# Kernel optimization log

Hardware: AMD Instinct MI355X
Metric: run time of the kernel (lower is better)

## Reference

```python
import jax, jax.numpy as jnp
import numpy as np

DIM = 512
HEADS = 8
DIM_HEAD = 64
BLOCKS = 6
EXCHANGES = 3
EPS = 1.1920929e-07  # torch.finfo(float32).eps used by RMSNorm(eps=None)


def _rmsnorm(x, w):
    return x * jax.lax.rsqrt(jnp.mean(x * x, axis=-1, keepdims=True) + EPS) * w


def _attention(x, ctx, nw, wq, wkv, wo):
    # x: [B, i, d] queries; ctx: [B, j, d] context (NOT normalized, as in original)
    B = x.shape[0]
    xn = _rmsnorm(x, nw)
    q = jnp.einsum('bid,ed->bie', xn, wq)
    kv = jnp.einsum('bjd,ed->bje', ctx, wkv)
    k, v = jnp.split(kv, 2, axis=-1)
    heads = lambda t: t.reshape(B, t.shape[1], HEADS, DIM_HEAD).transpose(0, 2, 1, 3)
    q, k, v = heads(q), heads(k), heads(v)
    sim = jnp.einsum('bhid,bhjd->bhij', q, k)  # NOTE: original never applies self.scale
    attn = jax.nn.softmax(sim, axis=-1)
    out = jnp.einsum('bhij,bhjd->bhid', attn, v)
    out = out.transpose(0, 2, 1, 3).reshape(B, -1, HEADS * DIM_HEAD)
    return jnp.einsum('bie,de->bid', out, wo)


def _feedforward(x, nw, kw, kb, vw, vb):
    q = _rmsnorm(x, nw)
    h = jnp.einsum('...d,ed->...e', q, kw) + kb
    sim, gates = jnp.split(h, 2, axis=-1)
    h = sim * jax.nn.gelu(gates, approximate=False)  # F.gelu default = exact erf
    return jnp.einsum('...e,de->...d', h, vw) + vb


def _forward(tokens, attn_norm_w, attn_wq, attn_wkv, attn_wo,
             ff_norm_w, ff_keys_w, ff_keys_b, ff_values_w, ff_values_b,
             res_norm_w, res_wq, res_wkv, res_wo):
    b, n, d = tokens.shape
    tokens = jnp.broadcast_to(tokens[None], (BLOCKS, b, n, d))
    messages = [tokens]
    for _ in range(EXCHANGES):
        flat = tokens.reshape(BLOCKS * b, n, d)
        attended = _attention(flat, flat, attn_norm_w, attn_wq, attn_wkv, attn_wo)
        attended = attended.reshape(BLOCKS, b, n, d)
        retrieved = _feedforward(tokens, ff_norm_w, ff_keys_w, ff_keys_b, ff_values_w, ff_values_b)
        messages += [attended, retrieved]
        packed = jnp.concatenate(messages, axis=0)           # [M, b, n, d]
        M = packed.shape[0]
        # einops: repeat 'm b n d -> (b blocks) n m d'
        ctx = jnp.broadcast_to(packed.transpose(1, 2, 0, 3)[:, None], (b, BLOCKS, n, M, d))
        ctx = ctx.reshape(b * BLOCKS * n, M, d)
        # queries packed '(blocks b) n d' then '* n d' -> [blocks*b*n, 1, d]
        q = tokens.reshape(BLOCKS * b * n, 1, d)
        pooled = _attention(q, ctx, res_norm_w, res_wq, res_wkv, res_wo)
        tokens = pooled.reshape(BLOCKS, b, n, d)
    return tokens


def setup_inputs() -> dict:
    key = jax.random.key(0)
    ks = jax.random.split(key, 12)
    b, n, d = 2, 256, DIM
    di = HEADS * DIM_HEAD
    dff = int(d * 4.0 * 2 / 3)
    s = lambda k, shp, fan: (jax.random.normal(k, shp, jnp.float32) / np.sqrt(fan)).astype(jnp.float32)
    return {
        'tokens': jax.random.normal(ks[0], (b, n, d), jnp.float32),
        'attn_norm_w': 1.0 + 0.05 * jax.random.normal(ks[1], (d,), jnp.float32),
        'attn_wq': s(ks[2], (di, d), d),
        'attn_wkv': s(ks[3], (2 * di, d), d),
        'attn_wo': s(ks[4], (d, di), di),
        'ff_norm_w': 1.0 + 0.05 * jax.random.normal(ks[5], (d,), jnp.float32),
        'ff_keys_w': s(ks[6], (2 * dff, d), d),
        'ff_keys_b': 0.01 * jax.random.normal(ks[7], (2 * dff,), jnp.float32),
        'ff_values_w': s(ks[8], (d, dff), dff),
        'ff_values_b': 0.01 * jax.random.normal(ks[9], (d,), jnp.float32),
        'res_norm_w': 1.0 + 0.05 * jax.random.normal(ks[10], (d,), jnp.float32),
        'res_wq': s(ks[11], (di, d), d),
        'res_wkv': s(jax.random.fold_in(key, 100), (2 * di, d), d),
        'res_wo': s(jax.random.fold_in(key, 101), (d, di), di),
    }


def reference(tokens, attn_norm_w, attn_wq, attn_wkv, attn_wo,
              ff_norm_w, ff_keys_w, ff_keys_b, ff_values_w, ff_values_b,
              res_norm_w, res_wq, res_wkv, res_wo):
    return _forward(tokens, attn_norm_w, attn_wq, attn_wkv, attn_wo,
                    ff_norm_w, ff_keys_w, ff_keys_b, ff_values_w, ff_values_b,
                    res_norm_w, res_wq, res_wkv, res_wo)
```

## Files before the change

kernel.cpp:

```cpp
#include <hip/hip_runtime.h>
#include <math.h>

#define Dm   512
#define Nn_  256
#define Bv   2
#define NTD  1024
#define NH   8
#define DH   64
#define DFF  1365
#define DFF2 2730
#define KFF  1408
#define NFF  2816
#define NMD  14
#define EPSR 1.1920929e-07f

typedef _Float16 h16;
typedef h16  v8h  __attribute__((ext_vector_type(8)));
typedef float v4f __attribute__((ext_vector_type(4)));

__device__ inline h16 f2h(float v) { return (h16)v; }

__device__ inline void glds16(const void* g, void* l) {
    __builtin_amdgcn_global_load_lds((const __attribute__((address_space(1))) void*)g,
                                     (__attribute__((address_space(3))) void*)l, 16, 0, 0);
}

struct GDesc {
    const h16* A;
    const h16* W;
    const float* bias;
    float* C;
    h16* Cbf;
    long Apl, Wpl, bfpl;
    int lda, ldw, ldc, Nd, mbase, K, mode, nbx;
};

template <int BM>
__global__ __launch_bounds__(256) void mega_gemm(GDesc d0, GDesc d1, GDesc d2, GDesc d3,
                                                 int n0, int n01, int n012)
{
    constexpr int MI = BM / 32;
    constexpr int ASEG = BM / 16;
    constexpr int NSEG = 2 * ASEG + 16;
    constexpr int BUF = 2 * BM * 32 + 2 * 4096;
    constexpr int AH = 0, AL = BM * 32, WH = 2 * BM * 32, WL = 2 * BM * 32 + 4096;
    __shared__ h16 lds[2 * BUF];

    GDesc d; int lb = blockIdx.x;
    if (lb < n0) d = d0;
    else if (lb < n01) { d = d1; lb -= n0; }
    else if (lb < n012) { d = d2; lb -= n01; }
    else { d = d3; lb -= n012; }
    const int bx = lb % d.nbx;
    const int by = lb / d.nbx;

    const int tid = threadIdx.x;
    const int wid = tid >> 6;
    const int lane = tid & 63;
    const int wm = wid >> 1, wn = wid & 1;
    const int row16 = lane & 15, quad = lane >> 4;
    const long i0 = (long)bx * BM;
    const long j0 = (long)by * 128;
    const int l4 = lane >> 2;
    const int l2s = ((lane & 3) ^ (l4 & 3)) * 8;
    const int ksw = (quad ^ (row16 & 3)) * 8;

    auto stage = [&](int k0, h16* buf) {
        #pragma unroll
        for (int s = 0; s < NSEG / 4; ++s) {
            const int sg = wid * (NSEG / 4) + s;
            const h16* src;
            int dst;
            if (sg < ASEG) {
                src = d.A + (i0 + sg * 16 + l4) * (long)d.lda + k0 + l2s;
                dst = AH + sg * 512;
            } else if (sg < 2 * ASEG) {
                const int r = sg - ASEG;
                src = d.A + d.Apl + (i0 + r * 16 + l4) * (long)d.lda + k0 + l2s;
                dst = AL + r * 512;
            } else if (sg < 2 * ASEG + 8) {
                const int r = sg - 2 * ASEG;
                src = d.W + (j0 + r * 16 + l4) * (long)d.ldw + k0 + l2s;
                dst = WH + r * 512;
            } else {
                const int r = sg - 2 * ASEG - 8;
                src = d.W + d.Wpl + (j0 + r * 16 + l4) * (long)d.ldw + k0 + l2s;
                dst = WL + r * 512;
            }
            glds16(src, &buf[dst]);
        }
    };

    v4f acc[MI][4];
    #pragma unroll
    for (int a = 0; a < MI; ++a)
        #pragma unroll
        for (int b = 0; b < 4; ++b) acc[a][b] = (v4f){0.f, 0.f, 0.f, 0.f};

    stage(0, lds);
    int cur = 0;
    for (int k0 = 0; k0 < d.K; k0 += 32) {
        __syncthreads();
        h16* cbuf = &lds[cur * BUF];
        if (k0 + 32 < d.K) stage(k0 + 32, &lds[(cur ^ 1) * BUF]);

        v8h af[MI], al[MI];
        #pragma unroll
        for (int mi = 0; mi < MI; ++mi) {
            const int aoff = (wm * (BM / 2) + mi * 16 + row16) * 32 + ksw;
            af[mi] = *(const v8h*)&cbuf[AH + aoff];
            al[mi] = *(const v8h*)&cbuf[AL + aoff];
        }
        #pragma unroll
        for (int nj = 0; nj < 4; ++nj) {
            const int boff = (wn * 64 + nj * 16 + row16) * 32 + ksw;
            v8h bh = *(const v8h*)&cbuf[WH + boff];
            v8h bl = *(const v8h*)&cbuf[WL + boff];
            #pragma unroll
            for (int mi = 0; mi < MI; ++mi) {
                acc[mi][nj] = __builtin_amdgcn_mfma_f32_16x16x32_f16(af[mi], bh, acc[mi][nj], 0, 0, 0);
                acc[mi][nj] = __builtin_amdgcn_mfma_f32_16x16x32_f16(af[mi], bl, acc[mi][nj], 0, 0, 0);
                acc[mi][nj] = __builtin_amdgcn_mfma_f32_16x16x32_f16(al[mi], bh, acc[mi][nj], 0, 0, 0);
            }
        }
        cur ^= 1;
    }

    #pragma unroll
    for (int nj = 0; nj < 4; ++nj) {
        const int col = (int)j0 + wn * 64 + nj * 16 + row16;
        if (col < d.Nd) {
            const float bv = d.bias ? d.bias[col] : 0.f;
            #pragma unroll
            for (int mi = 0; mi < MI; ++mi) {
                #pragma unroll
                for (int r = 0; r < 4; ++r) {
                    const long row = i0 + wm * (BM / 2) + mi * 16 + quad * 4 + r;
                    const float v = acc[mi][nj][r] + bv;
                    if (d.mode == 0) {
                        d.C[row * (long)d.ldc + col] = v;
                    } else if (d.mode == 1) {
                        const long idx = row * (long)d.ldc + col;
                        const h16 hi = f2h(v);
                        d.Cbf[idx] = hi; d.Cbf[idx + d.bfpl] = f2h(v - (float)hi);
                    } else if (d.mode == 2) {
                        const long idx = row * (long)d.ldc + col;
                        d.C[idx] = v;
                        const h16 hi = f2h(v);
                        d.Cbf[idx] = hi; d.Cbf[idx + d.bfpl] = f2h(v - (float)hi);
                    } else if (d.mode == 3) {
                        const int rr = (int)row & 1023;
                        const int md = d.mbase * 2 + (rr >> 9);
                        const long orow = (long)(((rr >> 8) & 1) * 256 + (rr & 255)) * NMD + md;
                        d.C[orow * 1024 + col] = v;
                    } else if (d.mode == 4) {
                        const h16 hi = f2h(v);
                        const h16 lo = f2h(v - (float)hi);
                        if (col < 512) {
                            const long idx = row * 512 + col;
                            d.Cbf[idx] = hi; d.Cbf[idx + d.bfpl] = lo;
                        } else {
                            const int c = col - 512;
                            const int bh_ = ((int)(row >> 8)) * 8 + (c >> 6);
                            const long idx = (((long)bh_ * 64 + (c & 63)) << 8) + (row & 255);
                            h16* vtp = (h16*)d.C;
                            vtp[idx] = hi; vtp[idx + d.bfpl] = lo;
                        }
                    } else {
                        const int g = (int)(row >> 9), bb = ((int)row >> 8) & 1, nn = (int)row & 255;
                        #pragma unroll
                        for (int rep = 0; rep < 3; ++rep) {
                            const long orow = (long)(((g * 3 + rep) * 2 + bb) * 256 + nn);
                            d.C[orow * (long)d.ldc + col] = v;
                        }
                    }
                }
            }
        }
    }
}

__global__ void cvt_hilo(const float* __restrict__ x, int Ms, int Ks, int Kp,
                         h16* __restrict__ y, long plane, int total)
{
    const int idx = blockIdx.x * 256 + threadIdx.x;
    if (idx >= total) return;
    const int row = idx / Kp;
    const int col = idx - row * Kp;
    const float v = (row < Ms && col < Ks) ? x[(long)row * Ks + col] : 0.f;
    const h16 hi = f2h(v);
    y[idx] = hi;
    y[idx + plane] = f2h(v - (float)hi);
}

__global__ void cvt_hilo_T(const float* __restrict__ x, int R, int C,
                           h16* __restrict__ y, long plane, int total)
{
    const int idx = blockIdx.x * 256 + threadIdx.x;
    if (idx >= total) return;
    const int row = idx / R;
    const int col = idx - row * R;
    const float v = (row < C) ? x[(long)col * C + row] : 0.f;
    const h16 hi = f2h(v);
    y[idx] = hi;
    y[idx + plane] = f2h(v - (float)hi);
}

__global__ void fold_bias(const float* __restrict__ wkv, const float* __restrict__ b,
                          float* __restrict__ out)
{
    const int n = blockIdx.x * 256 + threadIdx.x;
    if (n >= 1024) return;
    float s = 0.f;
    const float* row = wkv + (long)n * 512;
    for (int d2 = 0; d2 < 512; ++d2) s = fmaf(row[d2], b[d2], s);
    out[n] = s;
}

__global__ __launch_bounds__(256) void rmsnorm3_bf(
    const float* __restrict__ x,
    const float* __restrict__ w0, const float* __restrict__ w1,
    const float* __restrict__ w2,
    h16* __restrict__ y0, h16* __restrict__ y1,
    h16* __restrict__ y2, long plane)
{
    const int r = blockIdx.x;
    const float* xr = x + (long)r * Dm;
    const int t = threadIdx.x;
    const float a = xr[t];
    const float b = xr[t + 256];
    float ss = a * a + b * b;
    #pragma unroll
    for (int off = 32; off > 0; off >>= 1) ss += __shfl_xor(ss, off, 64);
    __shared__ float w4[4];
    if ((t & 63) == 0) w4[t >> 6] = ss;
    __syncthreads();
    const float rs = rsqrtf((w4[0] + w4[1] + w4[2] + w4[3]) * (1.f / 512.f) + EPSR);
    const float na = a * rs, nb = b * rs;
    const long ia = (long)r * Dm + t, ib = ia + 256;
    h16 h;
    float v;
    v = na * w0[t];       h = f2h(v); y0[ia] = h; y0[ia + plane] = f2h(v - (float)h);
    v = nb * w0[t + 256]; h = f2h(v); y0[ib] = h; y0[ib + plane] = f2h(v - (float)h);
    v = na * w1[t];       h = f2h(v); y1[ia] = h; y1[ia + plane] = f2h(v - (float)h);
    v = nb * w1[t + 256]; h = f2h(v); y1[ib] = h; y1[ib + plane] = f2h(v - (float)h);
    v = na * w2[t];       h = f2h(v); y2[ia] = h; y2[ia + plane] = f2h(v - (float)h);
    v = nb * w2[t + 256]; h = f2h(v); y2[ib] = h; y2[ib + plane] = f2h(v - (float)h);
}

__global__ __launch_bounds__(256) void attn_glu(
    const h16* __restrict__ qhl, const h16* __restrict__ khl,
    const h16* __restrict__ vtb, long pl, h16* __restrict__ outbf,
    const float* __restrict__ hbuf, h16* __restrict__ hbf, long hpl)
{
    if (blockIdx.x >= 128) {
        const int r = blockIdx.x - 128;
        const float* row = hbuf + (long)r * NFF;
        for (int c = threadIdx.x; c < KFF; c += 256) {
            float v = 0.f;
            if (c < DFF) {
                const float sim = row[c];
                const float g = row[c + DFF];
                v = sim * (0.5f * g * (1.f + erff(g * 0.70710678118654752440f)));
            }
            const long idx = (long)r * KFF + c;
            const h16 hi = f2h(v);
            hbf[idx] = hi;
            hbf[idx + hpl] = f2h(v - (float)hi);
        }
        return;
    }

    __shared__ h16 kh[4096], kl[4096], vh[4096], vl[4096];
    __shared__ h16 pH[4 * 1024], pL[4 * 1024];

    const int bat = blockIdx.x >> 5;
    const int head = (blockIdx.x >> 2) & 7;
    const int qc = blockIdx.x & 3;
    const int t = threadIdx.x;
    const int w = t >> 6, lane = t & 63;
    const int row16 = lane & 15, quad = lane >> 4;

    v8h qh[2], ql[2];
    {
        const long qrow = (long)bat * 256 + qc * 64 + w * 16 + row16;
        const h16* qp = qhl + qrow * 512 + head * 64 + quad * 8;
        qh[0] = *(const v8h*)qp;        qh[1] = *(const v8h*)(qp + 32);
        ql[0] = *(const v8h*)(qp + pl); ql[1] = *(const v8h*)(qp + pl + 32);
    }

    v4f O[4];
    #pragma unroll
    for (int i = 0; i < 4; ++i) O[i] = (v4f){0.f, 0.f, 0.f, 0.f};
    float m[4] = {-1e30f, -1e30f, -1e30f, -1e30f};
    float l[4] = {0.f, 0.f, 0.f, 0.f};

    const int sj = t >> 3;
    const int sc = t & 7;
    const long kbase = ((long)bat * 256) * 512 + head * 64;
    const long vbase = ((long)(bat * 8 + head) * 64) << 8;

    for (int jc = 0; jc < 256; jc += 64) {
        __syncthreads();
        #pragma unroll
        for (int rep = 0; rep < 2; ++rep) {
            const int row = sj + rep * 32;
            const int dsw = row * 64 + ((sc ^ (row & 7)) * 8);
            const h16* ks = khl + kbase + (long)(jc + row) * 512 + sc * 8;
            const h16* vs = vtb + vbase + ((long)row << 8) + jc + sc * 8;
            *(v8h*)&kh[dsw] = *(const v8h*)ks;
            *(v8h*)&kl[dsw] = *(const v8h*)(ks + pl);
            *(v8h*)&vh[dsw] = *(const v8h*)vs;
            *(v8h*)&vl[dsw] = *(const v8h*)(vs + pl);
        }
        __syncthreads();

        v4f S[4];
        #pragma unroll
        for (int i = 0; i < 4; ++i) S[i] = (v4f){0.f, 0.f, 0.f, 0.f};
        #pragma unroll
        for (int kk = 0; kk < 2; ++kk) {
            #pragma unroll
            for (int tile = 0; tile < 4; ++tile) {
                const int off = (tile * 16 + row16) * 64 + (((kk * 4 + quad) ^ (row16 & 7)) * 8);
                v8h bh = *(const v8h*)&kh[off];
                v8h bl = *(const v8h*)&kl[off];
                S[tile] = __builtin_amdgcn_mfma_f32_16x16x32_f16(qh[kk], bh, S[tile], 0, 0, 0);
                S[tile] = __builtin_amdgcn_mfma_f32_16x16x32_f16(qh[kk], bl, S[tile], 0, 0, 0);
                S[tile] = __builtin_amdgcn_mfma_f32_16x16x32_f16(ql[kk], bh, S[tile], 0, 0, 0);
            }
        }

        float mc[4], sums[4], alpha[4];
        #pragma unroll
        for (int r = 0; r < 4; ++r) {
            float v = fmaxf(fmaxf(S[0][r], S[1][r]), fmaxf(S[2][r], S[3][r]));
            v = fmaxf(v, __shfl_xor(v, 1, 64));
            v = fmaxf(v, __shfl_xor(v, 2, 64));
            v = fmaxf(v, __shfl_xor(v, 4, 64));
            v = fmaxf(v, __shfl_xor(v, 8, 64));
            mc[r] = v;
        }
        #pragma unroll
        for (int r = 0; r < 4; ++r) {
            const float mn = fmaxf(m[r], mc[r]);
            alpha[r] = __expf(m[r] - mn);
            m[r] = mn;
            sums[r] = 0.f;
        }
        #pragma unroll
        for (int tile = 0; tile < 4; ++tile) {
            #pragma unroll
            for (int r = 0; r < 4; ++r) {
                const float p = __expf(S[tile][r] - m[r]);
                S[tile][r] = p;
                sums[r] += p;
            }
        }
        #pragma unroll
        for (int r = 0; r < 4; ++r) {
            float v = sums[r];
            v += __shfl_xor(v, 1, 64);
            v += __shfl_xor(v, 2, 64);
            v += __shfl_xor(v, 4, 64);
            v += __shfl_xor(v, 8, 64);
            l[r] = l[r] * alpha[r] + v;
        }
        #pragma unroll
        for (int tile = 0; tile < 4; ++tile)
            #pragma unroll
            for (int r = 0; r < 4; ++r) O[tile][r] *= alpha[r];

        #pragma unroll
        for (int tile = 0; tile < 4; ++tile) {
            const int chunkcol = tile * 2 + (row16 >> 3);
            #pragma unroll
            for (int r = 0; r < 4; ++r) {
                const int prow = quad * 4 + r;
                const int addr = w * 1024 + prow * 64 +
                                 ((chunkcol ^ (prow & 7)) * 8) + (row16 & 7);
                const float p = S[tile][r];
                const h16 hi = f2h(p);
                pH[addr] = hi;
                pL[addr] = f2h(p - (float)hi);
            }
        }

        #pragma unroll
        for (int kk = 0; kk < 2; ++kk) {
            const int poff = w * 1024 + row16 * 64 + (((kk * 4 + quad) ^ (row16 & 7)) * 8);
            v8h pa = *(const v8h*)&pH[poff];
            v8h pb = *(const v8h*)&pL[poff];
            #pragma unroll
            for (int tile = 0; tile < 4; ++tile) {
                const int off = (tile * 16 + row16) * 64 + (((kk * 4 + quad) ^ (row16 & 7)) * 8);
                v8h vbh = *(const v8h*)&vh[off];
                v8h vbl = *(const v8h*)&vl[off];
                O[tile] = __builtin_amdgcn_mfma_f32_16x16x32_f16(pa, vbh, O[tile], 0, 0, 0);
                O[tile] = __builtin_amdgcn_mfma_f32_16x16x32_f16(pa, vbl, O[tile], 0, 0, 0);
                O[tile] = __builtin_amdgcn_mfma_f32_16x16x32_f16(pb, vbh, O[tile], 0, 0, 0);
            }
        }
    }

    #pragma unroll
    for (int tile = 0; tile < 4; ++tile) {
        const int dim = tile * 16 + row16;
        #pragma unroll
        for (int r = 0; r < 4; ++r) {
            const long grow = (long)bat * 256 + qc * 64 + w * 16 + quad * 4 + r;
            const float v = O[tile][r] / l[r];
            const long idx = grow * 512 + head * 64 + dim;
            const h16 hi = f2h(v);
            outbf[idx] = hi;
            outbf[idx + pl] = f2h(v - (float)hi);
        }
    }
}

template <int M>
__global__ __launch_bounds__(128) void attn_pool_kernel(
    const float* __restrict__ qb, const float* __restrict__ kvc3,
    h16* __restrict__ outbf, long plane)
{
    const int rb = blockIdx.x >> 3;
    const int h = blockIdx.x & 7;
    __shared__ float k_lds[M * 66];
    __shared__ float v_lds[M * 66];
    __shared__ float q_lds[2 * 64];
    __shared__ float p_lds[2 * 64];
    const int t = threadIdx.x;
    const int g = rb >> 8, nn = rb & 255;

    for (int idx = t; idx < M * 64; idx += 128) {
        const int m = idx >> 6, d = idx & 63;
        const long base = ((long)rb * NMD + m) * 1024 + h * DH + d;
        k_lds[m * 66 + d] = kvc3[base];
        v_lds[m * 66 + d] = kvc3[base + 512];
    }
    {
        const int w = t >> 6, dd = t & 63;
        const long iq = (long)(g * 2 + w) * 256 + nn;
        q_lds[t] = qb[iq * Dm + h * DH + dd];
    }
    __syncthreads();

    const int w = t >> 6;
    const int lane = t & 63;
    float s = -1e30f;
    if (lane < M) {
        s = 0.f;
        const float* kr = &k_lds[lane * 66];
        const float* qr = &q_lds[w * 64];
        #pragma unroll
        for (int dd = 0; dd < 64; dd += 2) {
            s = fmaf(qr[dd], kr[dd], s);
            s = fmaf(qr[dd + 1], kr[dd + 1], s);
        }
    }
    float mx = s;
    #pragma unroll
    for (int off = 32; off > 0; off >>= 1) mx = fmaxf(mx, __shfl_xor(mx, off, 64));
    const float p = __expf(s - mx);
    float l = p;
    #pragma unroll
    for (int off = 32; off > 0; off >>= 1) l += __shfl_xor(l, off, 64);
    p_lds[w * 64 + lane] = p / l;

    float o = 0.f;
    const float* pr = &p_lds[w * 64];
    #pragma unroll
    for (int m = 0; m < M; ++m)
        o = fmaf(pr[m], v_lds[m * 66 + lane], o);

    const long iq = (long)(g * 2 + w) * 256 + nn;
    const long oidx = iq * Dm + h * DH + lane;
    const h16 hi = f2h(o);
    outbf[oidx] = hi;
    outbf[oidx + plane] = f2h(o - (float)hi);
}

__global__ void replicate_kernel(const float* __restrict__ src,
                                 float* __restrict__ tokens,
                                 h16* __restrict__ tokbf, long tpl)
{
    const int idx = blockIdx.x * blockDim.x + threadIdx.x;
    if (idx >= NTD * Dm) return;
    const float v = src[idx & (Bv * Nn_ * Dm - 1)];
    tokens[idx] = v;
    const h16 hi = f2h(v);
    tokbf[idx] = hi;
    tokbf[idx + tpl] = f2h(v - (float)hi);
}

extern "C" void kernel_launch(void* const* d_in, const int* in_sizes, int n_in,
                              void* d_out, int out_size, void* d_ws, size_t ws_size,
                              hipStream_t stream)
{
    const float* tok_in       = (const float*)d_in[0];
    const float* attn_norm_w  = (const float*)d_in[1];
    const float* attn_wq      = (const float*)d_in[2];
    const float* attn_wkv     = (const float*)d_in[3];
    const float* attn_wo      = (const float*)d_in[4];
    const float* ff_norm_w    = (const float*)d_in[5];
    const float* ff_keys_w    = (const float*)d_in[6];
    const float* ff_keys_b    = (const float*)d_in[7];
    const float* ff_values_w  = (const float*)d_in[8];
    const float* ff_values_b  = (const float*)d_in[9];
    const float* res_norm_w   = (const float*)d_in[10];
    const float* res_wq       = (const float*)d_in[11];
    const float* res_wkv      = (const float*)d_in[12];
    const float* res_wo       = (const float*)d_in[13];

    float* ws = (float*)d_ws;
    float* kvc3   = ws;
    float* tokens = kvc3 + 512L * NMD * 1024;
    float* qbuf   = tokens + (long)NTD * Dm;
    float* hbuf   = qbuf + (long)NTD * Dm;
    float* biasWf = hbuf + (long)NTD * NFF;

    h16* us = (h16*)(biasWf + 1024);
    const long apl = (long)NTD * Dm;
    const long hpl = (long)NTD * KFF;
    const long vtpl = (long)NTD * Dm;
    const long w1 = 512L * 512, w2 = 1024L * 512, w3 = (long)NFF * 512;
    const long w5 = (long)KFF * 512;
    const long wa_pl = 1024L * 512;
    const long wf_pl = 1024L * KFF;
    h16* tokbf = us; us += 2 * apl;
    h16* xa    = us; us += 2 * apl;
    h16* xf    = us; us += 2 * apl;
    h16* xr    = us; us += 2 * apl;
    h16* abf   = us; us += 2 * apl;
    h16* hbf   = us; us += 2 * hpl;
    h16* qhl   = us; us += 2 * apl;
    h16* khl   = us; us += 2 * apl;
    h16* vtb   = us; us += 2 * vtpl;
    h16* wqb   = us; us += 2 * w1;
    h16* wkvb  = us; us += 2 * w2;
    h16* fkb   = us; us += 2 * w3;
    h16* rqb   = us; us += 2 * w1;
    h16* rkvb  = us; us += 2 * w2;
    h16* rob   = us; us += 2 * w1;
    h16* woTb  = us; us += 2 * w1;
    h16* fvwTb = us; us += 2 * w5;
    h16* Wab   = us; us += 2 * wa_pl;
    h16* Wfb   = us; us += 2 * wf_pl;

    auto cvtw = [&](const float* src, int Ms, int Ks, int Kp, int Mpad,
                    h16* dst, long pl) {
        const int tot = Mpad * Kp;
        cvt_hilo<<<(tot + 255) / 256, 256, 0, stream>>>(src, Ms, Ks, Kp, dst, pl, tot);
    };
    cvtw(attn_wq,   512,  512, 512, 512,  wqb,  w1);
    cvtw(attn_wkv,  1024, 512, 512, 1024, wkvb, w2);
    cvtw(ff_keys_w, DFF2, 512, 512, NFF,  fkb,  w3);
    cvtw(res_wq,    512,  512, 512, 512,  rqb,  w1);
    cvtw(res_wkv,   1024, 512, 512, 1024, rkvb, w2);
    cvtw(res_wo,    512,  512, 512, 512,  rob,  w1);
    cvt_hilo_T<<<(512 * 512 + 255) / 256, 256, 0, stream>>>(attn_wo, 512, 512, woTb, w1, 512 * 512);
    cvt_hilo_T<<<((int)w5 + 255) / 256, 256, 0, stream>>>(ff_values_w, 512, DFF, fvwTb, w5, (int)w5);
    fold_bias<<<4, 256, 0, stream>>>(res_wkv, ff_values_b, biasWf);

    auto mk = [](const h16* A, long Apl, int lda,
                 const h16* W, long Wpl, int ldw,
                 const float* bias, float* C, int ldc, int Nd,
                 h16* Cbf, long bfpl, int mbase, int K,
                 int mode, int nbx) -> GDesc {
        GDesc d;
        d.A = A; d.Apl = Apl; d.lda = lda;
        d.W = W; d.Wpl = Wpl; d.ldw = ldw;
        d.bias = bias; d.C = C; d.ldc = ldc; d.Nd = Nd;
        d.Cbf = Cbf; d.bfpl = bfpl; d.mbase = mbase; d.K = K;
        d.mode = mode; d.nbx = nbx;
        return d;
    };

    {
        GDesc dWf = mk(rkvb, w2, 512, fvwTb, w5, 512, nullptr, nullptr, KFF, KFF,
                       Wfb, wf_pl, 0, 512, 1, 16);
        GDesc dWa = mk(rkvb, w2, 512, woTb, w1, 512, nullptr, nullptr, 512, 512,
                       Wab, wa_pl, 0, 512, 1, 16);
        mega_gemm<64><<<240, 256, 0, stream>>>(dWf, dWa, dWa, dWa, 176, 240, 240);
    }

    replicate_kernel<<<(NTD * Dm + 255) / 256, 256, 0, stream>>>(tok_in, tokens, tokbf, apl);

    for (int e = 0; e < 3; ++e) {
        rmsnorm3_bf<<<NTD, 256, 0, stream>>>(tokens, attn_norm_w, ff_norm_w, res_norm_w,
                                             xa, xf, xr, apl);
        {
            GDesc dffk = mk(xf,    apl, 512, fkb,  w3, 512, ff_keys_b, hbuf, NFF, DFF2,
                            nullptr, 0, 0, 512, 0, 16);
            GDesc dwkv = mk(tokbf, apl, 512, wkvb, w2, 512, nullptr, (float*)vtb, 1024, 1024,
                            khl, apl, 0, 512, 4, 16);
            GDesc dwq  = mk(xa,    apl, 512, wqb,  w1, 512, nullptr, nullptr, 512, 512,
                            qhl, apl, 0, 512, 1, 16);
            mega_gemm<64><<<544, 256, 0, stream>>>(dffk, dwkv, dwq, dwq, 352, 480, 544);
        }
        attn_glu<<<1152, 256, 0, stream>>>(qhl, khl, vtb, apl, abf, hbuf, hbf, hpl);
        {
            GDesc dffvKV = mk(hbf, hpl, KFF, Wfb, wf_pl, KFF, biasWf, kvc3, 1024, 1024,
                              nullptr, 0, 2 + 2 * e, KFF, 3, 16);
            GDesc dwoKV  = mk(abf, apl, 512, Wab, wa_pl, 512, nullptr, kvc3, 1024, 1024,
                              nullptr, 0, 1 + 2 * e, 512, 3, 16);
            GDesc drq    = mk(xr, apl, 512, rqb, w1, 512, nullptr, qbuf, 512, 512,
                              nullptr, 0, 0, 512, 0, 16);
            if (e == 0) {
                GDesc dtokKV = mk(tokbf, apl, 512, rkvb, w2, 512, nullptr, kvc3, 1024, 1024,
                                  nullptr, 0, 0, 512, 3, 16);
                mega_gemm<64><<<448, 256, 0, stream>>>(dffvKV, dwoKV, drq, dtokKV, 128, 256, 320);
            } else {
                mega_gemm<64><<<320, 256, 0, stream>>>(dffvKV, dwoKV, drq, drq, 128, 256, 320);
            }
        }
        if (e == 0)      attn_pool_kernel<6><<<512 * NH, 128, 0, stream>>>(qbuf, kvc3, abf, apl);
        else if (e == 1) attn_pool_kernel<10><<<512 * NH, 128, 0, stream>>>(qbuf, kvc3, abf, apl);
        else             attn_pool_kernel<14><<<512 * NH, 128, 0, stream>>>(qbuf, kvc3, abf, apl);
        {
            if (e < 2) {
                GDesc dro = mk(abf, apl, 512, rob, w1, 512, nullptr, tokens, 512, 512,
                               tokbf, apl, 0, 512, 2, 32);
                mega_gemm<32><<<128, 256, 0, stream>>>(dro, dro, dro, dro, 128, 128, 128);
            } else {
                GDesc dro = mk(abf, apl, 512, rob, w1, 512, nullptr, (float*)d_out, 512, 512,
                               nullptr, 0, 0, 512, 5, 32);
                mega_gemm<32><<<128, 256, 0, stream>>>(dro, dro, dro, dro, 128, 128, 128);
            }
        }
    }
}
```

Baseline: 490.4 us.

## Fold RMSNorm weights into weights, fuse setup kernels, add BN=64 GEMM tiles

The RMSNorm gain vectors are folded into the converted query and FF-key weights. The per-row rsqrt scale is now applied in the GEMM epilogue from a small rs_kernel output, so the three normalized hi/lo activation buffers no longer need to be written and read each exchange. All weight conversion, bias folding and token replication kernels are merged into one setup launch. The GEMM gains a BN template parameter, and most launches use 64x64 tiles with twice as many blocks, which raises parallelism at the cost of reloading the A tile more often.

```diff
diff --git a/kernel.cpp b/kernel.cpp
--- a/kernel.cpp
+++ b/kernel.cpp
@@ -29,21 +29,26 @@
     const h16* A;
     const h16* W;
     const float* bias;
+    const float* rss;
     float* C;
     h16* Cbf;
     long Apl, Wpl, bfpl;
     int lda, ldw, ldc, Nd, mbase, K, mode, nbx;
 };
 
-template <int BM>
+template <int BM, int BN>
 __global__ __launch_bounds__(256) void mega_gemm(GDesc d0, GDesc d1, GDesc d2, GDesc d3,
                                                  int n0, int n01, int n012)
 {
-    constexpr int MI = BM / 32;
+    constexpr int NWN = (BN == 128) ? 2 : 1;
+    constexpr int NWM = 4 / NWN;
+    constexpr int MI = BM / (16 * NWM);
+    constexpr int ABUF = BM * 32;
+    constexpr int WBUFh = BN * 32;
+    constexpr int BUF = 2 * ABUF + 2 * WBUFh;
     constexpr int ASEG = BM / 16;
-    constexpr int NSEG = 2 * ASEG + 16;
-    constexpr int BUF = 2 * BM * 32 + 2 * 4096;
-    constexpr int AH = 0, AL = BM * 32, WH = 2 * BM * 32, WL = 2 * BM * 32 + 4096;
+    constexpr int WSEG = BN / 16;
+    constexpr int NSEG = 2 * ASEG + 2 * WSEG;
     __shared__ h16 lds[2 * BUF];
 
     GDesc d; int lb = blockIdx.x;
@@ -57,10 +62,10 @@
     const int tid = threadIdx.x;
     const int wid = tid >> 6;
     const int lane = tid & 63;
-    const int wm = wid >> 1, wn = wid & 1;
+    const int wm = wid / NWN, wn = wid % NWN;
     const int row16 = lane & 15, quad = lane >> 4;
     const long i0 = (long)bx * BM;
-    const long j0 = (long)by * 128;
+    const long j0 = (long)by * BN;
     const int l4 = lane >> 2;
     const int l2s = ((lane & 3) ^ (l4 & 3)) * 8;
     const int ksw = (quad ^ (row16 & 3)) * 8;
@@ -73,19 +78,19 @@
             int dst;
             if (sg < ASEG) {
                 src = d.A + (i0 + sg * 16 + l4) * (long)d.lda + k0 + l2s;
-                dst = AH + sg * 512;
+                dst = sg * 512;
             } else if (sg < 2 * ASEG) {
                 const int r = sg - ASEG;
                 src = d.A + d.Apl + (i0 + r * 16 + l4) * (long)d.lda + k0 + l2s;
-                dst = AL + r * 512;
-            } else if (sg < 2 * ASEG + 8) {
+                dst = ABUF + r * 512;
+            } else if (sg < 2 * ASEG + WSEG) {
                 const int r = sg - 2 * ASEG;
                 src = d.W + (j0 + r * 16 + l4) * (long)d.ldw + k0 + l2s;
-                dst = WH + r * 512;
+                dst = 2 * ABUF + r * 512;
             } else {
-                const int r = sg - 2 * ASEG - 8;
+                const int r = sg - 2 * ASEG - WSEG;
                 src = d.W + d.Wpl + (j0 + r * 16 + l4) * (long)d.ldw + k0 + l2s;
-                dst = WL + r * 512;
+                dst = 2 * ABUF + WBUFh + r * 512;
             }
             glds16(src, &buf[dst]);
         }
@@ -107,15 +112,15 @@
         v8h af[MI], al[MI];
         #pragma unroll
         for (int mi = 0; mi < MI; ++mi) {
-            const int aoff = (wm * (BM / 2) + mi * 16 + row16) * 32 + ksw;
-            af[mi] = *(const v8h*)&cbuf[AH + aoff];
-            al[mi] = *(const v8h*)&cbuf[AL + aoff];
+            const int aoff = (wm * (16 * MI) + mi * 16 + row16) * 32 + ksw;
+            af[mi] = *(const v8h*)&cbuf[aoff];
+            al[mi] = *(const v8h*)&cbuf[ABUF + aoff];
         }
         #pragma unroll
         for (int nj = 0; nj < 4; ++nj) {
             const int boff = (wn * 64 + nj * 16 + row16) * 32 + ksw;
-            v8h bh = *(const v8h*)&cbuf[WH + boff];
-            v8h bl = *(const v8h*)&cbuf[WL + boff];
+            v8h bh = *(const v8h*)&cbuf[2 * ABUF + boff];
+            v8h bl = *(const v8h*)&cbuf[2 * ABUF + WBUFh + boff];
             #pragma unroll
             for (int mi = 0; mi < MI; ++mi) {
                 acc[mi][nj] = __builtin_amdgcn_mfma_f32_16x16x32_f16(af[mi], bh, acc[mi][nj], 0, 0, 0);
@@ -135,8 +140,10 @@
             for (int mi = 0; mi < MI; ++mi) {
                 #pragma unroll
                 for (int r = 0; r < 4; ++r) {
-                    const long row = i0 + wm * (BM / 2) + mi * 16 + quad * 4 + r;
-                    const float v = acc[mi][nj][r] + bv;
+                    const long row = i0 + wm * (16 * MI) + mi * 16 + quad * 4 + r;
+                    float v = acc[mi][nj][r];
+                    if (d.rss) v *= d.rss[(int)row];
+                    v += bv;
                     if (d.mode == 0) {
                         d.C[row * (long)d.ldc + col] = v;
                     } else if (d.mode == 1) {
@@ -180,24 +187,29 @@
     }
 }
 
-__global__ void cvt_hilo(const float* __restrict__ x, int Ms, int Ks, int Kp,
-                         h16* __restrict__ y, long plane, int total)
-{
-    const int idx = blockIdx.x * 256 + threadIdx.x;
-    if (idx >= total) return;
+struct SetupP {
+    const float *attn_wq, *attn_wkv, *ff_keys_w, *res_wq, *res_wkv, *res_wo,
+                *attn_wo, *ff_values_w, *ff_values_b,
+                *attn_norm_w, *ff_norm_w, *res_norm_w, *tok_in;
+    h16 *wqb, *wkvb, *fkb, *rqb, *rkvb, *rob, *woTb, *fvwTb, *tokbf;
+    float *biasWf, *tokens;
+};
+
+__device__ inline void cvt_dev(int idx, const float* x, int Ms, int Ks, int Kp,
+                               h16* y, long plane, const float* cs)
+{
     const int row = idx / Kp;
     const int col = idx - row * Kp;
-    const float v = (row < Ms && col < Ks) ? x[(long)row * Ks + col] : 0.f;
+    float v = (row < Ms && col < Ks) ? x[(long)row * Ks + col] : 0.f;
+    if (cs) v *= cs[col];
     const h16 hi = f2h(v);
     y[idx] = hi;
     y[idx + plane] = f2h(v - (float)hi);
 }
 
-__global__ void cvt_hilo_T(const float* __restrict__ x, int R, int C,
-                           h16* __restrict__ y, long plane, int total)
-{
-    const int idx = blockIdx.x * 256 + threadIdx.x;
-    if (idx >= total) return;
+__device__ inline void cvtT_dev(int idx, const float* x, int R, int C,
+                                h16* y, long plane)
+{
     const int row = idx / R;
     const int col = idx - row * R;
     const float v = (row < C) ? x[(long)col * C + row] : 0.f;
@@ -206,46 +218,63 @@
     y[idx + plane] = f2h(v - (float)hi);
 }
 
-__global__ void fold_bias(const float* __restrict__ wkv, const float* __restrict__ b,
-                          float* __restrict__ out)
-{
-    const int n = blockIdx.x * 256 + threadIdx.x;
-    if (n >= 1024) return;
-    float s = 0.f;
-    const float* row = wkv + (long)n * 512;
-    for (int d2 = 0; d2 < 512; ++d2) s = fmaf(row[d2], b[d2], s);
-    out[n] = s;
-}
-
-__global__ __launch_bounds__(256) void rmsnorm3_bf(
-    const float* __restrict__ x,
-    const float* __restrict__ w0, const float* __restrict__ w1,
-    const float* __restrict__ w2,
-    h16* __restrict__ y0, h16* __restrict__ y1,
-    h16* __restrict__ y2, long plane)
-{
-    const int r = blockIdx.x;
-    const float* xr = x + (long)r * Dm;
+__global__ __launch_bounds__(256) void setup_all(SetupP p)
+{
+    long b = blockIdx.x;
     const int t = threadIdx.x;
-    const float a = xr[t];
-    const float b = xr[t + 256];
-    float ss = a * a + b * b;
+    if (b < 1024) { cvt_dev((int)(b * 256 + t), p.attn_wq, 512, 512, 512, p.wqb, 512L * 512, p.attn_norm_w); return; }
+    b -= 1024;
+    if (b < 2048) { cvt_dev((int)(b * 256 + t), p.attn_wkv, 1024, 512, 512, p.wkvb, 1024L * 512, nullptr); return; }
+    b -= 2048;
+    if (b < 5632) { cvt_dev((int)(b * 256 + t), p.ff_keys_w, DFF2, 512, 512, p.fkb, (long)NFF * 512, p.ff_norm_w); return; }
+    b -= 5632;
+    if (b < 1024) { cvt_dev((int)(b * 256 + t), p.res_wq, 512, 512, 512, p.rqb, 512L * 512, p.res_norm_w); return; }
+    b -= 1024;
+    if (b < 2048) { cvt_dev((int)(b * 256 + t), p.res_wkv, 1024, 512, 512, p.rkvb, 1024L * 512, nullptr); return; }
+    b -= 2048;
+    if (b < 1024) { cvt_dev((int)(b * 256 + t), p.res_wo, 512, 512, 512, p.rob, 512L * 512, nullptr); return; }
+    b -= 1024;
+    if (b < 1024) { cvtT_dev((int)(b * 256 + t), p.attn_wo, 512, 512, p.woTb, 512L * 512); return; }
+    b -= 1024;
+    if (b < 2816) { cvtT_dev((int)(b * 256 + t), p.ff_values_w, 512, DFF, p.fvwTb, (long)KFF * 512); return; }
+    b -= 2816;
+    if (b < 4) {
+        const int n = (int)(b * 256 + t);
+        if (n < 1024) {
+            float s = 0.f;
+            const float* row = p.res_wkv + (long)n * 512;
+            for (int dd = 0; dd < 512; ++dd) s = fmaf(row[dd], p.ff_values_b[dd], s);
+            p.biasWf[n] = s;
+        }
+        return;
+    }
+    b -= 4;
+    {
+        const int idx = (int)(b * 256 + t);
+        const float v = p.tok_in[idx & (Bv * Nn_ * Dm - 1)];
+        p.tokens[idx] = v;
+        const h16 hi = f2h(v);
+        p.tokbf[idx] = hi;
+        p.tokbf[idx + (long)NTD * Dm] = f2h(v - (float)hi);
+    }
+}
+#define SETUP_BLOCKS 18692
+
+__global__ __launch_bounds__(256) void rs_kernel(const float* __restrict__ x,
+                                                 float* __restrict__ rs)
+{
+    const int r = blockIdx.x * 4 + (threadIdx.x >> 6);
+    const int lane = threadIdx.x & 63;
+    const float* row = x + (long)r * Dm + lane * 8;
+    float ss = 0.f;
+    #pragma unroll
+    for (int i = 0; i < 8; i += 4) {
+        const float4 v = *(const float4*)(row + i);
+        ss += v.x * v.x + v.y * v.y + v.z * v.z + v.w * v.w;
+    }
     #pragma unroll
     for (int off = 32; off > 0; off >>= 1) ss += __shfl_xor(ss, off, 64);
-    __shared__ float w4[4];
-    if ((t & 63) == 0) w4[t >> 6] = ss;
-    __syncthreads();
-    const float rs = rsqrtf((w4[0] + w4[1] + w4[2] + w4[3]) * (1.f / 512.f) + EPSR);
-    const float na = a * rs, nb = b * rs;
-    const long ia = (long)r * Dm + t, ib = ia + 256;
-    h16 h;
-    float v;
-    v = na * w0[t];       h = f2h(v); y0[ia] = h; y0[ia + plane] = f2h(v - (float)h);
-    v = nb * w0[t + 256]; h = f2h(v); y0[ib] = h; y0[ib + plane] = f2h(v - (float)h);
-    v = na * w1[t];       h = f2h(v); y1[ia] = h; y1[ia + plane] = f2h(v - (float)h);
-    v = nb * w1[t + 256]; h = f2h(v); y1[ib] = h; y1[ib + plane] = f2h(v - (float)h);
-    v = na * w2[t];       h = f2h(v); y2[ia] = h; y2[ia + plane] = f2h(v - (float)h);
-    v = nb * w2[t + 256]; h = f2h(v); y2[ib] = h; y2[ib + plane] = f2h(v - (float)h);
+    if (lane == 0) rs[r] = rsqrtf(ss * (1.f / 512.f) + EPSR);
 }
 
 __global__ __launch_bounds__(256) void attn_glu(
@@ -478,19 +507,6 @@
     const h16 hi = f2h(o);
     outbf[oidx] = hi;
     outbf[oidx + plane] = f2h(o - (float)hi);
-}
-
-__global__ void replicate_kernel(const float* __restrict__ src,
-                                 float* __restrict__ tokens,
-                                 h16* __restrict__ tokbf, long tpl)
-{
-    const int idx = blockIdx.x * blockDim.x + threadIdx.x;
-    if (idx >= NTD * Dm) return;
-    const float v = src[idx & (Bv * Nn_ * Dm - 1)];
-    tokens[idx] = v;
-    const h16 hi = f2h(v);
-    tokbf[idx] = hi;
-    tokbf[idx + tpl] = f2h(v - (float)hi);
 }
 
 extern "C" void kernel_launch(void* const* d_in, const int* in_sizes, int n_in,
@@ -518,24 +534,21 @@
     float* qbuf   = tokens + (long)NTD * Dm;
     float* hbuf   = qbuf + (long)NTD * Dm;
     float* biasWf = hbuf + (long)NTD * NFF;
-
-    h16* us = (h16*)(biasWf + 1024);
+    float* rsbuf  = biasWf + 1024;
+
+    h16* us = (h16*)(rsbuf + 1024);
     const long apl = (long)NTD * Dm;
     const long hpl = (long)NTD * KFF;
-    const long vtpl = (long)NTD * Dm;
     const long w1 = 512L * 512, w2 = 1024L * 512, w3 = (long)NFF * 512;
     const long w5 = (long)KFF * 512;
     const long wa_pl = 1024L * 512;
     const long wf_pl = 1024L * KFF;
     h16* tokbf = us; us += 2 * apl;
-    h16* xa    = us; us += 2 * apl;
-    h16* xf    = us; us += 2 * apl;
-    h16* xr    = us; us += 2 * apl;
     h16* abf   = us; us += 2 * apl;
     h16* hbf   = us; us += 2 * hpl;
     h16* qhl   = us; us += 2 * apl;
     h16* khl   = us; us += 2 * apl;
-    h16* vtb   = us; us += 2 * vtpl;
+    h16* vtb   = us; us += 2 * apl;
     h16* wqb   = us; us += 2 * w1;
     h16* wkvb  = us; us += 2 * w2;
     h16* fkb   = us; us += 2 * w3;
@@ -547,71 +560,67 @@
     h16* Wab   = us; us += 2 * wa_pl;
     h16* Wfb   = us; us += 2 * wf_pl;
 
-    auto cvtw = [&](const float* src, int Ms, int Ks, int Kp, int Mpad,
-                    h16* dst, long pl) {
-        const int tot = Mpad * Kp;
-        cvt_hilo<<<(tot + 255) / 256, 256, 0, stream>>>(src, Ms, Ks, Kp, dst, pl, tot);
-    };
-    cvtw(attn_wq,   512,  512, 512, 512,  wqb,  w1);
-    cvtw(attn_wkv,  1024, 512, 512, 1024, wkvb, w2);
-    cvtw(ff_keys_w, DFF2, 512, 512, NFF,  fkb,  w3);
-    cvtw(res_wq,    512,  512, 512, 512,  rqb,  w1);
-    cvtw(res_wkv,   1024, 512, 512, 1024, rkvb, w2);
-    cvtw(res_wo,    512,  512, 512, 512,  rob,  w1);
-    cvt_hilo_T<<<(512 * 512 + 255) / 256, 256, 0, stream>>>(attn_wo, 512, 512, woTb, w1, 512 * 512);
-    cvt_hilo_T<<<((int)w5 + 255) / 256, 256, 0, stream>>>(ff_values_w, 512, DFF, fvwTb, w5, (int)w5);
-    fold_bias<<<4, 256, 0, stream>>>(res_wkv, ff_values_b, biasWf);
+    {
+        SetupP p;
+        p.attn_wq = attn_wq; p.attn_wkv = attn_wkv; p.ff_keys_w = ff_keys_w;
+        p.res_wq = res_wq; p.res_wkv = res_wkv; p.res_wo = res_wo;
+        p.attn_wo = attn_wo; p.ff_values_w = ff_values_w; p.ff_values_b = ff_values_b;
+        p.attn_norm_w = attn_norm_w; p.ff_norm_w = ff_norm_w; p.res_norm_w = res_norm_w;
+        p.tok_in = tok_in;
+        p.wqb = wqb; p.wkvb = wkvb; p.fkb = fkb; p.rqb = rqb; p.rkvb = rkvb;
+        p.rob = rob; p.woTb = woTb; p.fvwTb = fvwTb; p.tokbf = tokbf;
+        p.biasWf = biasWf; p.tokens = tokens;
+        setup_all<<<SETUP_BLOCKS, 256, 0, stream>>>(p);
+    }
 
     auto mk = [](const h16* A, long Apl, int lda,
                  const h16* W, long Wpl, int ldw,
-                 const float* bias, float* C, int ldc, int Nd,
+                 const float* bias, const float* rss,
+                 float* C, int ldc, int Nd,
                  h16* Cbf, long bfpl, int mbase, int K,
                  int mode, int nbx) -> GDesc {
         GDesc d;
         d.A = A; d.Apl = Apl; d.lda = lda;
         d.W = W; d.Wpl = Wpl; d.ldw = ldw;
-        d.bias = bias; d.C = C; d.ldc = ldc; d.Nd = Nd;
+        d.bias = bias; d.rss = rss; d.C = C; d.ldc = ldc; d.Nd = Nd;
         d.Cbf = Cbf; d.bfpl = bfpl; d.mbase = mbase; d.K = K;
         d.mode = mode; d.nbx = nbx;
         return d;
     };
 
     {
-        GDesc dWf = mk(rkvb, w2, 512, fvwTb, w5, 512, nullptr, nullptr, KFF, KFF,
+        GDesc dWf = mk(rkvb, w2, 512, fvwTb, w5, 512, nullptr, nullptr, nullptr, KFF, KFF,
                        Wfb, wf_pl, 0, 512, 1, 16);
-        GDesc dWa = mk(rkvb, w2, 512, woTb, w1, 512, nullptr, nullptr, 512, 512,
+        GDesc dWa = mk(rkvb, w2, 512, woTb, w1, 512, nullptr, nullptr, nullptr, 512, 512,
                        Wab, wa_pl, 0, 512, 1, 16);
-        mega_gemm<64><<<240, 256, 0, stream>>>(dWf, dWa, dWa, dWa, 176, 240, 240);
-    }
-
-    replicate_kernel<<<(NTD * Dm + 255) / 256, 256, 0, stream>>>(tok_in, tokens, tokbf, apl);
+        mega_gemm<64, 64><<<480, 256, 0, stream>>>(dWf, dWa, dWa, dWa, 352, 480, 480);
+    }
 
     for (int e = 0; e < 3; ++e) {
-        rmsnorm3_bf<<<NTD, 256, 0, stream>>>(tokens, attn_norm_w, ff_norm_w, res_norm_w,
-                                             xa, xf, xr, apl);
+        rs_kernel<<<256, 256, 0, stream>>>(tokens, rsbuf);
         {
-            GDesc dffk = mk(xf,    apl, 512, fkb,  w3, 512, ff_keys_b, hbuf, NFF, DFF2,
+            GDesc dffk = mk(tokbf, apl, 512, fkb,  w3, 512, ff_keys_b, rsbuf, hbuf, NFF, DFF2,
                             nullptr, 0, 0, 512, 0, 16);
-            GDesc dwkv = mk(tokbf, apl, 512, wkvb, w2, 512, nullptr, (float*)vtb, 1024, 1024,
+            GDesc dwkv = mk(tokbf, apl, 512, wkvb, w2, 512, nullptr, nullptr, (float*)vtb, 1024, 1024,
                             khl, apl, 0, 512, 4, 16);
-            GDesc dwq  = mk(xa,    apl, 512, wqb,  w1, 512, nullptr, nullptr, 512, 512,
+            GDesc dwq  = mk(tokbf, apl, 512, wqb,  w1, 512, nullptr, rsbuf, nullptr, 512, 512,
                             qhl, apl, 0, 512, 1, 16);
-            mega_gemm<64><<<544, 256, 0, stream>>>(dffk, dwkv, dwq, dwq, 352, 480, 544);
+            mega_gemm<64, 64><<<1088, 256, 0, stream>>>(dffk, dwkv, dwq, dwq, 704, 960, 1088);
         }
         attn_glu<<<1152, 256, 0, stream>>>(qhl, khl, vtb, apl, abf, hbuf, hbf, hpl);
         {
-            GDesc dffvKV = mk(hbf, hpl, KFF, Wfb, wf_pl, KFF, biasWf, kvc3, 1024, 1024,
+            GDesc dffvKV = mk(hbf, hpl, KFF, Wfb, wf_pl, KFF, biasWf, nullptr, kvc3, 1024, 1024,
                               nullptr, 0, 2 + 2 * e, KFF, 3, 16);
-            GDesc dwoKV  = mk(abf, apl, 512, Wab, wa_pl, 512, nullptr, kvc3, 1024, 1024,
+            GDesc dwoKV  = mk(abf, apl, 512, Wab, wa_pl, 512, nullptr, nullptr, kvc3, 1024, 1024,
                               nullptr, 0, 1 + 2 * e, 512, 3, 16);
-            GDesc drq    = mk(xr, apl, 512, rqb, w1, 512, nullptr, qbuf, 512, 512,
+            GDesc drq    = mk(tokbf, apl, 512, rqb, w1, 512, nullptr, rsbuf, qbuf, 512, 512,
                               nullptr, 0, 0, 512, 0, 16);
             if (e == 0) {
-                GDesc dtokKV = mk(tokbf, apl, 512, rkvb, w2, 512, nullptr, kvc3, 1024, 1024,
+                GDesc dtokKV = mk(tokbf, apl, 512, rkvb, w2, 512, nullptr, nullptr, kvc3, 1024, 1024,
                                   nullptr, 0, 0, 512, 3, 16);
-                mega_gemm<64><<<448, 256, 0, stream>>>(dffvKV, dwoKV, drq, dtokKV, 128, 256, 320);
+                mega_gemm<64, 64><<<896, 256, 0, stream>>>(dffvKV, dwoKV, drq, dtokKV, 256, 512, 640);
             } else {
-                mega_gemm<64><<<320, 256, 0, stream>>>(dffvKV, dwoKV, drq, drq, 128, 256, 320);
+                mega_gemm<64, 64><<<640, 256, 0, stream>>>(dffvKV, dwoKV, drq, drq, 256, 512, 640);
             }
         }
         if (e == 0)      attn_pool_kernel<6><<<512 * NH, 128, 0, stream>>>(qbuf, kvc3, abf, apl);
@@ -619,14 +628,14 @@
         else             attn_pool_kernel<14><<<512 * NH, 128, 0, stream>>>(qbuf, kvc3, abf, apl);
         {
             if (e < 2) {
-                GDesc dro = mk(abf, apl, 512, rob, w1, 512, nullptr, tokens, 512, 512,
+                GDesc dro = mk(abf, apl, 512, rob, w1, 512, nullptr, nullptr, tokens, 512, 512,
                                tokbf, apl, 0, 512, 2, 32);
-                mega_gemm<32><<<128, 256, 0, stream>>>(dro, dro, dro, dro, 128, 128, 128);
+                mega_gemm<32, 128><<<128, 256, 0, stream>>>(dro, dro, dro, dro, 128, 128, 128);
             } else {
-                GDesc dro = mk(abf, apl, 512, rob, w1, 512, nullptr, (float*)d_out, 512, 512,
+                GDesc dro = mk(abf, apl, 512, rob, w1, 512, nullptr, nullptr, (float*)d_out, 512, 512,
                                nullptr, 0, 0, 512, 5, 32);
-                mega_gemm<32><<<128, 256, 0, stream>>>(dro, dro, dro, dro, 128, 128, 128);
-            }
-        }
-    }
-}
+                mega_gemm<32, 128><<<128, 256, 0, stream>>>(dro, dro, dro, dro, 128, 128, 128);
+            }
+        }
+    }
+}
```

After: 467.0 us. -4.8%, faster.
